# Optimization experiments

Measured on AMD Instinct MI355X. Metric: run time of the kernel, lower is better.

The kernel has to match this reference:

```python
import jax, jax.numpy as jnp
import numpy as np

N = 100000
E = 600000
H = 128
L = 2  # mp_ngcn


def setup_inputs() -> dict:
    key = jax.random.key(0)
    k = jax.random.split(key, 8)
    h = jax.random.normal(k[0], (N, H), dtype=jnp.float32)
    edge_row = jax.random.randint(k[1], (E,), 0, N, dtype=jnp.int32)
    edge_col = jax.random.randint(k[2], (E,), 0, N, dtype=jnp.int32)
    edge_w = jax.random.uniform(k[3], (E,), dtype=jnp.float32)
    # xavier_normal gain=1.414 for square fc: std = 1.414*sqrt(2/(H+H))
    std = 1.414 * np.sqrt(2.0 / (H + H))
    fc_w = jax.random.normal(k[4], (L, H, H), dtype=jnp.float32) * std
    fc_b = jnp.zeros((L, H), dtype=jnp.float32)           # init 0.0
    gcn_bias = jnp.full((L, H), 0.001, dtype=jnp.float32)  # init 0.001
    prelu_a = jnp.full((L,), 0.25, dtype=jnp.float32)      # PReLU default
    return {"h": h, "edge_row": edge_row, "edge_col": edge_col,
            "edge_w": edge_w, "fc_w": fc_w, "fc_b": fc_b,
            "gcn_bias": gcn_bias, "prelu_a": prelu_a}


def reference(h, edge_row, edge_col, edge_w, fc_w, fc_b, gcn_bias, prelu_a):
    x = h
    for i in range(L):
        # dense linear transform: [N,H] @ [H,H]^T + b
        s = x @ fc_w[i].T + fc_b[i]
        # sparse adjacency spmm: out[r] = sum_e w_e * s[c_e]
        msg = s[edge_col] * edge_w[:, None]        # [E,H] gather + scale
        out = jax.ops.segment_sum(msg, edge_row, num_segments=N)
        out = out + gcn_bias[i]
        # dropout (eval-mode identity), then PReLU
        x = jnp.where(out > 0, out, prelu_a[i] * out)
    return x
```

## Files before the change

### kernel.cpp

```cpp
#include <hip/hip_runtime.h>

#define H 128

typedef __attribute__((ext_vector_type(8))) short bf16x8;
typedef __attribute__((ext_vector_type(4))) short s16x4;
typedef __attribute__((ext_vector_type(4))) float f32x4;

__device__ inline unsigned short f2bf(float f) {
    unsigned u = __float_as_uint(f);
    unsigned r = (u + 0x7fffu + ((u >> 16) & 1u)) >> 16;
    return (unsigned short)r;
}
__device__ inline float bflo(unsigned u) { return __uint_as_float(u << 16); }
__device__ inline float bfhi(unsigned u) { return __uint_as_float(u & 0xffff0000u); }

__device__ inline unsigned pack_cw(int c, float w) {
    unsigned q = (unsigned)(w * 32768.f);
    if (q > 32767u) q = 32767u;
    return ((unsigned)c << 15) | q;
}

#define MB 64

template<bool BF16IN>
__global__ __launch_bounds__(256) void gemm_mfma_kernel(
    const void* __restrict__ xv, const float* __restrict__ W,
    const float* __restrict__ b, short* __restrict__ s_out, int N, int nbatch)
{
    __shared__ short wlds[H * 136];

    const int t = threadIdx.x;
    const int l = t & 63;
    const int w = t >> 6;
    const int n_g   = (w & 1) * 32;
    const int col_g = (w >> 1) * 64;
    const int ln15 = l & 15;
    const int lhi  = l >> 4;

    #pragma unroll
    for (int i = 0; i < 16; ++i) {
        int fidx = i * 256 + t;
        int j  = fidx >> 5;
        int c4 = fidx & 31;
        float4 v = *reinterpret_cast<const float4*>(W + (size_t)j * H + c4 * 4);
        s16x4 p;
        p[0] = (short)f2bf(v.x); p[1] = (short)f2bf(v.y);
        p[2] = (short)f2bf(v.z); p[3] = (short)f2bf(v.w);
        *reinterpret_cast<s16x4*>(&wlds[j * 136 + c4 * 4]) = p;
    }

    float4 bias4[4];
    #pragma unroll
    for (int jt = 0; jt < 4; ++jt)
        bias4[jt] = *reinterpret_cast<const float4*>(b + col_g + jt * 16 + lhi * 4);

    __syncthreads();

    for (int batch = blockIdx.x; batch < nbatch; batch += gridDim.x) {
        const int row0 = batch * MB;

        bf16x8 ax[4][2];
        #pragma unroll
        for (int nf = 0; nf < 2; ++nf) {
            const int n = row0 + n_g + nf * 16 + ln15;
            const bool ok = (n < N);
            #pragma unroll
            for (int ks = 0; ks < 4; ++ks) {
                bf16x8 f = {0, 0, 0, 0, 0, 0, 0, 0};
                if (ok) {
                    if (BF16IN) {
                        f = *reinterpret_cast<const bf16x8*>(
                            (const short*)xv + (size_t)n * H + ks * 32 + lhi * 8);
                    } else {
                        const float* p = (const float*)xv + (size_t)n * H + ks * 32 + lhi * 8;
                        float4 lo = *reinterpret_cast<const float4*>(p);
                        float4 hi = *reinterpret_cast<const float4*>(p + 4);
                        f[0] = (short)f2bf(lo.x); f[1] = (short)f2bf(lo.y);
                        f[2] = (short)f2bf(lo.z); f[3] = (short)f2bf(lo.w);
                        f[4] = (short)f2bf(hi.x); f[5] = (short)f2bf(hi.y);
                        f[6] = (short)f2bf(hi.z); f[7] = (short)f2bf(hi.w);
                    }
                }
                ax[ks][nf] = f;
            }
        }

        f32x4 acc[2][4] = {};
        #pragma unroll
        for (int ks = 0; ks < 4; ++ks) {
            #pragma unroll
            for (int jt = 0; jt < 4; ++jt) {
                bf16x8 aw = *reinterpret_cast<const bf16x8*>(
                    &wlds[(col_g + jt * 16 + ln15) * 136 + ks * 32 + lhi * 8]);
                acc[0][jt] = __builtin_amdgcn_mfma_f32_16x16x32_bf16(
                    aw, ax[ks][0], acc[0][jt], 0, 0, 0);
                acc[1][jt] = __builtin_amdgcn_mfma_f32_16x16x32_bf16(
                    aw, ax[ks][1], acc[1][jt], 0, 0, 0);
            }
        }

        #pragma unroll
        for (int nf = 0; nf < 2; ++nf) {
            const int n = row0 + n_g + nf * 16 + ln15;
            if (n < N) {
                #pragma unroll
                for (int jt = 0; jt < 4; ++jt) {
                    s16x4 p;
                    p[0] = (short)f2bf(acc[nf][jt][0] + bias4[jt].x);
                    p[1] = (short)f2bf(acc[nf][jt][1] + bias4[jt].y);
                    p[2] = (short)f2bf(acc[nf][jt][2] + bias4[jt].z);
                    p[3] = (short)f2bf(acc[nf][jt][3] + bias4[jt].w);
                    *reinterpret_cast<s16x4*>(
                        s_out + (size_t)n * H + col_g + jt * 16 + lhi * 4) = p;
                }
            }
        }
    }
}

__global__ __launch_bounds__(256) void count_rank_kernel(
    const int* __restrict__ erow, int* __restrict__ counts,
    int* __restrict__ rank, int E)
{
    int e = blockIdx.x * blockDim.x + threadIdx.x;
    if (e < E) rank[e] = atomicAdd(&counts[erow[e]], 1);
}

#define SCAN_BLK 1024
__global__ __launch_bounds__(SCAN_BLK) void scan_block_kernel(
    const int* __restrict__ counts, int* __restrict__ incl,
    int* __restrict__ bsums, int N)
{
    __shared__ int sm[SCAN_BLK];
    int i = blockIdx.x * SCAN_BLK + threadIdx.x;
    int v = (i < N) ? counts[i] : 0;
    sm[threadIdx.x] = v;
    __syncthreads();
    for (int off = 1; off < SCAN_BLK; off <<= 1) {
        int tv = (threadIdx.x >= off) ? sm[threadIdx.x - off] : 0;
        __syncthreads();
        sm[threadIdx.x] += tv;
        __syncthreads();
    }
    if (i < N) incl[i] = sm[threadIdx.x];
    if (threadIdx.x == SCAN_BLK - 1) bsums[blockIdx.x] = sm[SCAN_BLK - 1];
}

__global__ __launch_bounds__(SCAN_BLK) void scan_sums_kernel(int* __restrict__ bsums, int nb)
{
    __shared__ int sm[SCAN_BLK];
    if (nb <= SCAN_BLK) {
        int i = threadIdx.x;
        int v = (i < nb) ? bsums[i] : 0;
        sm[i] = v;
        __syncthreads();
        for (int off = 1; off < SCAN_BLK; off <<= 1) {
            int tv = (i >= off) ? sm[i - off] : 0;
            __syncthreads();
            sm[i] += tv;
            __syncthreads();
        }
        if (i < nb) bsums[i] = sm[i] - v;
    } else if (threadIdx.x == 0) {
        int run = 0;
        for (int i = 0; i < nb; ++i) { int v = bsums[i]; bsums[i] = run; run += v; }
    }
}

__global__ __launch_bounds__(SCAN_BLK) void finalize_offsets_kernel(
    const int* __restrict__ counts, const int* __restrict__ incl,
    const int* __restrict__ bsums, int* __restrict__ offsets, int N, int E)
{
    int i = blockIdx.x * SCAN_BLK + threadIdx.x;
    if (i < N) offsets[i] = incl[i] - counts[i] + bsums[blockIdx.x];
    if (i == 0) offsets[N] = E;
}

__global__ __launch_bounds__(256) void fill_kernel(
    const int* __restrict__ erow, const int* __restrict__ ecol,
    const float* __restrict__ ew, const int* __restrict__ offsets,
    const int* __restrict__ rank, unsigned* __restrict__ cw, int E)
{
    int e = blockIdx.x * blockDim.x + threadIdx.x;
    if (e < E) {
        int r = erow[e];
        cw[offsets[r] + rank[e]] = pack_cw(ecol[e], ew[e]);
    }
}

template<int MODE>
__global__ __launch_bounds__(256) void spmm_csr2_kernel(
    const int* __restrict__ offsets, const unsigned* __restrict__ cw,
    const short* __restrict__ s_bf, const float* __restrict__ gbias,
    const float* __restrict__ a_ptr, float* __restrict__ out_f,
    short* __restrict__ out_b, int N)
{
    const float a = a_ptr[0];
    int gid = blockIdx.x * blockDim.x + threadIdx.x;
    int wid  = gid >> 6;
    int l    = gid & 63;
    int half = l >> 5;
    int li   = l & 31;
    int r = wid * 2 + half;
    if (r >= N) return;

    const int beg = offsets[r], end = offsets[r + 1];
    const size_t coff = (size_t)li * 4;
    const float SC = 1.f / 32768.f;

    float a00=0.f,a01=0.f,a02=0.f,a03=0.f;
    float a10=0.f,a11=0.f,a12=0.f,a13=0.f;
    float a20=0.f,a21=0.f,a22=0.f,a23=0.f;
    float a30=0.f,a31=0.f,a32=0.f,a33=0.f;

    int e = beg;
    for (; e + 4 <= end; e += 4) {
        unsigned p0 = cw[e],     p1 = cw[e + 1];
        unsigned p2 = cw[e + 2], p3 = cw[e + 3];
        float w0 = (float)(p0 & 0x7fffu) * SC;
        float w1 = (float)(p1 & 0x7fffu) * SC;
        float w2 = (float)(p2 & 0x7fffu) * SC;
        float w3 = (float)(p3 & 0x7fffu) * SC;
        unsigned long long u0 = *reinterpret_cast<const unsigned long long*>(
            s_bf + (size_t)(p0 >> 15) * H + coff);
        unsigned long long u1 = *reinterpret_cast<const unsigned long long*>(
            s_bf + (size_t)(p1 >> 15) * H + coff);
        unsigned long long u2 = *reinterpret_cast<const unsigned long long*>(
            s_bf + (size_t)(p2 >> 15) * H + coff);
        unsigned long long u3 = *reinterpret_cast<const unsigned long long*>(
            s_bf + (size_t)(p3 >> 15) * H + coff);
        unsigned lo;
        lo = (unsigned)u0; a00 += w0 * bflo(lo); a01 += w0 * bfhi(lo);
        lo = (unsigned)(u0 >> 32); a02 += w0 * bflo(lo); a03 += w0 * bfhi(lo);
        lo = (unsigned)u1; a10 += w1 * bflo(lo); a11 += w1 * bfhi(lo);
        lo = (unsigned)(u1 >> 32); a12 += w1 * bflo(lo); a13 += w1 * bfhi(lo);
        lo = (unsigned)u2; a20 += w2 * bflo(lo); a21 += w2 * bfhi(lo);
        lo = (unsigned)(u2 >> 32); a22 += w2 * bflo(lo); a23 += w2 * bfhi(lo);
        lo = (unsigned)u3; a30 += w3 * bflo(lo); a31 += w3 * bfhi(lo);
        lo = (unsigned)(u3 >> 32); a32 += w3 * bflo(lo); a33 += w3 * bfhi(lo);
    }
    for (; e < end; ++e) {
        unsigned p0 = cw[e];
        float w0 = (float)(p0 & 0x7fffu) * SC;
        unsigned long long u0 = *reinterpret_cast<const unsigned long long*>(
            s_bf + (size_t)(p0 >> 15) * H + coff);
        unsigned lo;
        lo = (unsigned)u0; a00 += w0 * bflo(lo); a01 += w0 * bfhi(lo);
        lo = (unsigned)(u0 >> 32); a02 += w0 * bflo(lo); a03 += w0 * bfhi(lo);
    }

    float4 g = *reinterpret_cast<const float4*>(gbias + li * 4);
    float v0 = (a00 + a10) + (a20 + a30) + g.x;
    float v1 = (a01 + a11) + (a21 + a31) + g.y;
    float v2 = (a02 + a12) + (a22 + a32) + g.z;
    float v3 = (a03 + a13) + (a23 + a33) + g.w;
    v0 = v0 > 0.f ? v0 : a * v0;
    v1 = v1 > 0.f ? v1 : a * v1;
    v2 = v2 > 0.f ? v2 : a * v2;
    v3 = v3 > 0.f ? v3 : a * v3;

    if (MODE == 0) {
        *reinterpret_cast<float4*>(out_f + (size_t)r * H + li * 4) =
            make_float4(v0, v1, v2, v3);
    } else {
        s16x4 p;
        p[0] = (short)f2bf(v0); p[1] = (short)f2bf(v1);
        p[2] = (short)f2bf(v2); p[3] = (short)f2bf(v3);
        *reinterpret_cast<s16x4*>(out_b + (size_t)r * H + li * 4) = p;
    }
}

__global__ __launch_bounds__(256) void init_out_kernel(
    float* __restrict__ out, const float* __restrict__ gbias, int total4)
{
    int i = blockIdx.x * blockDim.x + threadIdx.x;
    const int stride = gridDim.x * blockDim.x;
    for (; i < total4; i += stride) {
        int c4 = i & 31;
        float4 bv = *reinterpret_cast<const float4*>(gbias + c4 * 4);
        *reinterpret_cast<float4*>(out + (size_t)i * 4) = bv;
    }
}

__global__ __launch_bounds__(256) void spmm_edge_kernel(
    const int* __restrict__ erow, const int* __restrict__ ecol,
    const float* __restrict__ ew, const short* __restrict__ s_bf,
    float* __restrict__ out, int E)
{
    long long gid = (long long)blockIdx.x * blockDim.x + threadIdx.x;
    int e = (int)(gid >> 6);
    int l = (int)(gid & 63);
    if (e >= E) return;
    int r = erow[e];
    int c = ecol[e];
    float w = ew[e];
    unsigned u = *reinterpret_cast<const unsigned*>(s_bf + (size_t)c * H + 2 * l);
    unsafeAtomicAdd(out + (size_t)r * H + l * 2 + 0, bflo(u) * w);
    unsafeAtomicAdd(out + (size_t)r * H + l * 2 + 1, bfhi(u) * w);
}

__global__ __launch_bounds__(256) void prelu_kernel(
    float* __restrict__ buf, const float* __restrict__ a_ptr, int total4)
{
    const float a = a_ptr[0];
    int i = blockIdx.x * blockDim.x + threadIdx.x;
    const int stride = gridDim.x * blockDim.x;
    for (; i < total4; i += stride) {
        float4 v = *reinterpret_cast<float4*>(buf + (size_t)i * 4);
        v.x = v.x > 0.f ? v.x : a * v.x;
        v.y = v.y > 0.f ? v.y : a * v.y;
        v.z = v.z > 0.f ? v.z : a * v.z;
        v.w = v.w > 0.f ? v.w : a * v.w;
        *reinterpret_cast<float4*>(buf + (size_t)i * 4) = v;
    }
}

extern "C" void kernel_launch(void* const* d_in, const int* in_sizes, int n_in,
                              void* d_out, int out_size, void* d_ws, size_t ws_size,
                              hipStream_t stream)
{
    const float* h        = (const float*)d_in[0];
    const int*   erow     = (const int*)d_in[1];
    const int*   ecol     = (const int*)d_in[2];
    const float* ew       = (const float*)d_in[3];
    const float* fc_w     = (const float*)d_in[4];
    const float* fc_b     = (const float*)d_in[5];
    const float* gcn_bias = (const float*)d_in[6];
    const float* prelu_a  = (const float*)d_in[7];

    const int N = in_sizes[0] / H;
    const int E = in_sizes[1];
    float* out = (float*)d_out;

    char* ws = (char*)d_ws;
    short* s_bf  = (short*)ws;
    size_t off = (size_t)N * H * sizeof(short);
    short* x1_bf = (short*)(ws + off); off += (size_t)N * H * sizeof(short);
    int* counts  = (int*)(ws + off); off += (size_t)N * 4;
    int* incl    = (int*)(ws + off); off += (size_t)N * 4;
    int* offsets = (int*)(ws + off); off += (size_t)(N + 1) * 4;
    const int nb_scan = (N + SCAN_BLK - 1) / SCAN_BLK;
    int* bsums   = (int*)(ws + off); off += (size_t)nb_scan * 4;
    int* rank    = (int*)(ws + off); off += (size_t)E * 4;
    unsigned* cw = (unsigned*)(ws + off); off += (size_t)E * 4;

    const int eblocks = (E + 255) / 256;
    const int nbatch = (N + MB - 1) / MB;
    const int ggrid = nbatch < 1024 ? nbatch : 1024;

    if (off <= ws_size) {
        hipMemsetAsync(counts, 0, (size_t)N * 4, stream);
        count_rank_kernel<<<eblocks, 256, 0, stream>>>(erow, counts, rank, E);
        scan_block_kernel<<<nb_scan, SCAN_BLK, 0, stream>>>(counts, incl, bsums, N);
        scan_sums_kernel<<<1, SCAN_BLK, 0, stream>>>(bsums, nb_scan);
        finalize_offsets_kernel<<<nb_scan, SCAN_BLK, 0, stream>>>(
            counts, incl, bsums, offsets, N, E);
        fill_kernel<<<eblocks, 256, 0, stream>>>(erow, ecol, ew, offsets, rank, cw, E);

        const int spmm_blocks = (int)((((long long)(N + 1) / 2) * 64 + 255) / 256);

        gemm_mfma_kernel<false><<<ggrid, 256, 0, stream>>>(h, fc_w, fc_b, s_bf, N, nbatch);
        spmm_csr2_kernel<1><<<spmm_blocks, 256, 0, stream>>>(
            offsets, cw, s_bf, gcn_bias, prelu_a, nullptr, x1_bf, N);
        gemm_mfma_kernel<true><<<ggrid, 256, 0, stream>>>(
            x1_bf, fc_w + H * H, fc_b + H, s_bf, N, nbatch);
        spmm_csr2_kernel<0><<<spmm_blocks, 256, 0, stream>>>(
            offsets, cw, s_bf, gcn_bias + H, prelu_a + 1, out, nullptr, N);
    } else {
        const int total4 = N * (H / 4);
        const int spmm_blocks = (int)(((long long)E * 64 + 255) / 256);

        gemm_mfma_kernel<false><<<ggrid, 256, 0, stream>>>(h, fc_w, fc_b, s_bf, N, nbatch);
        init_out_kernel<<<2048, 256, 0, stream>>>(out, gcn_bias, total4);
        spmm_edge_kernel<<<spmm_blocks, 256, 0, stream>>>(erow, ecol, ew, s_bf, out, E);
        prelu_kernel<<<2048, 256, 0, stream>>>(out, prelu_a, total4);

        gemm_mfma_kernel<false><<<ggrid, 256, 0, stream>>>(out, fc_w + H * H, fc_b + H, s_bf, N, nbatch);
        init_out_kernel<<<2048, 256, 0, stream>>>(out, gcn_bias + H, total4);
        spmm_edge_kernel<<<spmm_blocks, 256, 0, stream>>>(erow, ecol, ew, s_bf, out, E);
        prelu_kernel<<<2048, 256, 0, stream>>>(out, prelu_a + 1, total4);
    }
}
```

Baseline: 163.8 us.

## Fuse edge counting with first GEMM and fold block-sum scan into finalize

```diff
diff --git a/kernel.cpp b/kernel.cpp
--- a/kernel.cpp
+++ b/kernel.cpp
@@ -23,12 +23,11 @@
 #define MB 64
 
 template<bool BF16IN>
-__global__ __launch_bounds__(256) void gemm_mfma_kernel(
-    const void* __restrict__ xv, const float* __restrict__ W,
-    const float* __restrict__ b, short* __restrict__ s_out, int N, int nbatch)
-{
-    __shared__ short wlds[H * 136];
-
+__device__ __forceinline__ void gemm_body(
+    short* wlds, const void* __restrict__ xv, const float* __restrict__ W,
+    const float* __restrict__ b, short* __restrict__ s_out, int N, int nbatch,
+    int bid, int grid)
+{
     const int t = threadIdx.x;
     const int l = t & 63;
     const int w = t >> 6;
@@ -56,7 +55,7 @@
 
     __syncthreads();
 
-    for (int batch = blockIdx.x; batch < nbatch; batch += gridDim.x) {
+    for (int batch = bid; batch < nbatch; batch += grid) {
         const int row0 = batch * MB;
 
         bf16x8 ax[4][2];
@@ -118,12 +117,36 @@
     }
 }
 
-__global__ __launch_bounds__(256) void count_rank_kernel(
+template<bool BF16IN>
+__global__ __launch_bounds__(256) void gemm_mfma_kernel(
+    const void* __restrict__ xv, const float* __restrict__ W,
+    const float* __restrict__ b, short* __restrict__ s_out, int N, int nbatch)
+{
+    __shared__ short wlds[H * 136];
+    gemm_body<BF16IN>(wlds, xv, W, b, s_out, N, nbatch, blockIdx.x, gridDim.x);
+}
+
+__global__ __launch_bounds__(256) void count_plus_gemm_kernel(
     const int* __restrict__ erow, int* __restrict__ counts,
-    int* __restrict__ rank, int E)
-{
-    int e = blockIdx.x * blockDim.x + threadIdx.x;
-    if (e < E) rank[e] = atomicAdd(&counts[erow[e]], 1);
+    int* __restrict__ rank, int E, int count_blocks,
+    const void* __restrict__ xv, const float* __restrict__ W,
+    const float* __restrict__ b, short* __restrict__ s_out, int N, int nbatch,
+    int gemm_grid)
+{
+    __shared__ short wlds[H * 136];
+    if ((int)blockIdx.x < count_blocks) {
+        int e = blockIdx.x * 256 + threadIdx.x;
+        if (e < E) rank[e] = atomicAdd(&counts[erow[e]], 1);
+        return;
+    }
+    gemm_body<false>(wlds, xv, W, b, s_out, N, nbatch,
+                     (int)blockIdx.x - count_blocks, gemm_grid);
+}
+
+__global__ __launch_bounds__(256) void zero_kernel(int4* __restrict__ p, int n4)
+{
+    int i = blockIdx.x * blockDim.x + threadIdx.x;
+    if (i < n4) p[i] = make_int4(0, 0, 0, 0);
 }
 
 #define SCAN_BLK 1024
@@ -146,33 +169,20 @@
     if (threadIdx.x == SCAN_BLK - 1) bsums[blockIdx.x] = sm[SCAN_BLK - 1];
 }
 
-__global__ __launch_bounds__(SCAN_BLK) void scan_sums_kernel(int* __restrict__ bsums, int nb)
-{
-    __shared__ int sm[SCAN_BLK];
-    if (nb <= SCAN_BLK) {
-        int i = threadIdx.x;
-        int v = (i < nb) ? bsums[i] : 0;
-        sm[i] = v;
-        __syncthreads();
-        for (int off = 1; off < SCAN_BLK; off <<= 1) {
-            int tv = (i >= off) ? sm[i - off] : 0;
-            __syncthreads();
-            sm[i] += tv;
-            __syncthreads();
-        }
-        if (i < nb) bsums[i] = sm[i] - v;
-    } else if (threadIdx.x == 0) {
-        int run = 0;
-        for (int i = 0; i < nb; ++i) { int v = bsums[i]; bsums[i] = run; run += v; }
-    }
-}
-
 __global__ __launch_bounds__(SCAN_BLK) void finalize_offsets_kernel(
     const int* __restrict__ counts, const int* __restrict__ incl,
-    const int* __restrict__ bsums, int* __restrict__ offsets, int N, int E)
-{
-    int i = blockIdx.x * SCAN_BLK + threadIdx.x;
-    if (i < N) offsets[i] = incl[i] - counts[i] + bsums[blockIdx.x];
+    const int* __restrict__ bsums, int* __restrict__ offsets, int N, int E, int nb)
+{
+    __shared__ int sb[SCAN_BLK];
+    int tid = threadIdx.x;
+    sb[tid] = (tid < nb) ? bsums[tid] : 0;
+    __syncthreads();
+    int prefix = 0;
+    const int bid = blockIdx.x;
+    for (int j = 0; j < bid; ++j) prefix += sb[j];
+
+    int i = bid * SCAN_BLK + tid;
+    if (i < N) offsets[i] = incl[i] - counts[i] + prefix;
     if (i == 0) offsets[N] = E;
 }
 
@@ -336,7 +346,8 @@
     short* s_bf  = (short*)ws;
     size_t off = (size_t)N * H * sizeof(short);
     short* x1_bf = (short*)(ws + off); off += (size_t)N * H * sizeof(short);
-    int* counts  = (int*)(ws + off); off += (size_t)N * 4;
+    off = (off + 15) & ~(size_t)15;
+    int* counts  = (int*)(ws + off); off += (size_t)((N + 3) & ~3) * 4;
     int* incl    = (int*)(ws + off); off += (size_t)N * 4;
     int* offsets = (int*)(ws + off); off += (size_t)(N + 1) * 4;
     const int nb_scan = (N + SCAN_BLK - 1) / SCAN_BLK;
@@ -349,17 +360,18 @@
     const int ggrid = nbatch < 1024 ? nbatch : 1024;
 
     if (off <= ws_size) {
-        hipMemsetAsync(counts, 0, (size_t)N * 4, stream);
-        count_rank_kernel<<<eblocks, 256, 0, stream>>>(erow, counts, rank, E);
+        const int n4 = (N + 3) / 4;
+        zero_kernel<<<(n4 + 255) / 256, 256, 0, stream>>>((int4*)counts, n4);
+        count_plus_gemm_kernel<<<eblocks + ggrid, 256, 0, stream>>>(
+            erow, counts, rank, E, eblocks,
+            h, fc_w, fc_b, s_bf, N, nbatch, ggrid);
         scan_block_kernel<<<nb_scan, SCAN_BLK, 0, stream>>>(counts, incl, bsums, N);
-        scan_sums_kernel<<<1, SCAN_BLK, 0, stream>>>(bsums, nb_scan);
         finalize_offsets_kernel<<<nb_scan, SCAN_BLK, 0, stream>>>(
-            counts, incl, bsums, offsets, N, E);
+            counts, incl, bsums, offsets, N, E, nb_scan);
         fill_kernel<<<eblocks, 256, 0, stream>>>(erow, ecol, ew, offsets, rank, cw, E);
 
         const int spmm_blocks = (int)((((long long)(N + 1) / 2) * 64 + 255) / 256);
 
-        gemm_mfma_kernel<false><<<ggrid, 256, 0, stream>>>(h, fc_w, fc_b, s_bf, N, nbatch);
         spmm_csr2_kernel<1><<<spmm_blocks, 256, 0, stream>>>(
             offsets, cw, s_bf, gcn_bias, prelu_a, nullptr, x1_bf, N);
         gemm_mfma_kernel<true><<<ggrid, 256, 0, stream>>>(
```

After: 157.8 us. -3.7%, faster.
